# Kernel tuning notes

Hardware: AMD Instinct MI355X
Metric: run time of the kernel (lower is better)

## Reference

```python
import jax, jax.numpy as jnp
import numpy as np

DEG = 3
KNOTS = np.array([i / 9.0 for i in range(1, 9)], dtype=np.float32)  # 8 knots in (0,1)
SDIM = DEG + 1 + len(KNOTS)  # 12
B, D_IN, D_HID, D_OUT = 32768, 256, 256, 1


def spline_basis(t):
    # TruncatedPowerBasis: [1, t, t^2, t^3, relu(t-k)^3 ...]  -> (B, SDIM)
    powers = t[:, None] ** jnp.arange(DEG + 1, dtype=t.dtype)
    knots = jnp.asarray(KNOTS, dtype=t.dtype)
    spl = jax.nn.relu(t[:, None] - knots[None, :]) ** DEG
    return jnp.concatenate([powers, spl], axis=1)


def vc_layer(x, basis, W, b, in_dim, out_dim):
    # Mathematically identical to torch: W_b = basis @ W (viewed (in,out)); out = x @ W_b + basis @ b
    # Factored to avoid materializing the (B, in, out) per-sample weight tensor.
    Ws = W.reshape(SDIM, in_dim, out_dim)
    tmp = jnp.einsum('bi,sio->bso', x, Ws)        # (B, SDIM, out)
    return jnp.einsum('bs,bso->bo', basis, tmp) + basis @ b


def setup_inputs() -> dict:
    key = jax.random.key(0)
    ks = jax.random.split(key, 8)
    xavier = lambda k, shape: jax.random.uniform(
        k, shape, dtype=jnp.float32,
        minval=-1.0, maxval=1.0) * np.sqrt(6.0 / (shape[0] + shape[1]))
    return {
        'treatment': jax.random.uniform(ks[0], (B,), dtype=jnp.float32),
        'features': jax.random.normal(ks[1], (B, D_IN), dtype=jnp.float32),
        'W0': xavier(ks[2], (SDIM, D_IN * D_HID)),
        'b0': xavier(ks[3], (SDIM, D_HID)),
        'W1': xavier(ks[4], (SDIM, D_HID * D_HID)),
        'b1': xavier(ks[5], (SDIM, D_HID)),
        'W2': xavier(ks[6], (SDIM, D_HID * D_OUT)),
        'b2': xavier(ks[7], (SDIM, D_OUT)),
    }


def reference(treatment, features, W0, b0, W1, b1, W2, b2):
    basis = spline_basis(treatment)                     # (B, SDIM)
    x = vc_layer(features, basis, W0, b0, D_IN, D_HID)
    x = jax.nn.relu(x)
    x = vc_layer(x, basis, W1, b1, D_HID, D_HID)
    x = jax.nn.relu(x)
    x = vc_layer(x, basis, W2, b2, D_HID, D_OUT)        # (B, 1)
    return x
```

## Files before the change

kernel.cpp:

```cpp
#include <hip/hip_runtime.h>


typedef __attribute__((ext_vector_type(8))) _Float16 half8;
typedef __attribute__((ext_vector_type(4))) _Float16 half4;
typedef __attribute__((ext_vector_type(4))) float floatx4;

#define XPAD 264

__device__ __forceinline__ void gload16(const _Float16* g, _Float16* l){
  __builtin_amdgcn_global_load_lds(
      (const __attribute__((address_space(1))) void*)g,
      (__attribute__((address_space(3))) void*)l, 16, 0, 0);
}

__device__ __forceinline__ void stage_b(const _Float16* wt, _Float16* slot,
                                        int w, int l){
  gload16(wt +        w * 512 + l * 8, slot +        w * 512);
  gload16(wt + 4096 + w * 512 + l * 8, slot + 4096 + w * 512);
}

__device__ __forceinline__ void make_basis(float t, float* p){
  p[0] = 1.f; p[1] = t; p[2] = t*t; p[3] = p[2]*t;
  const float knots[8] = {1.f/9.f, 2.f/9.f, 3.f/9.f, 4.f/9.f,
                          5.f/9.f, 6.f/9.f, 7.f/9.f, 8.f/9.f};
  #pragma unroll
  for (int j = 0; j < 8; ++j){
    float d = t - knots[j];
    d = fmaxf(d, 0.f);
    p[4+j] = d*d*d;
  }
}

__global__ __launch_bounds__(256)
void pack_w_kernel(const float* __restrict__ W0, const float* __restrict__ W1,
                   _Float16* __restrict__ Wp0, _Float16* __restrict__ Wp1){
  __shared__ float wl[32 * 260];
  const int blk = blockIdx.x;
  const float* W = (blk < 96) ? W0 : W1;
  _Float16* Wp   = (blk < 96) ? Wp0 : Wp1;
  const int c    = (blk < 96) ? blk : blk - 96;
  const int tid  = threadIdx.x;
  const float* src = W + (size_t)c * 8192;
  #pragma unroll
  for (int it = 0; it < 8; ++it){
    int idx = it * 256 + tid;
    int r = idx >> 6, c4 = idx & 63;
    float4 v = *(const float4*)(src + (size_t)idx * 4);
    float* d = &wl[r * 260 + c4 * 4];
    d[0] = v.x; d[1] = v.y; d[2] = v.z; d[3] = v.w;
  }
  __syncthreads();
  const int tpos = (c & 7) * 12 + (c >> 3);
  _Float16* dst = Wp + (size_t)tpos * 8192;
  #pragma unroll
  for (int w = 0; w < 4; ++w){
    int v = w * 256 + tid;
    int n16 = v & 15, qq = (v >> 4) & 3, ntg = v >> 6;
    half8 o;
    #pragma unroll
    for (int j = 0; j < 8; ++j)
      o[j] = (_Float16)wl[(qq * 8 + j) * 260 + ntg * 16 + n16];
    *(half8*)(dst + (size_t)v * 8) = o;
  }
}

__device__ __forceinline__ void gemm_kloop(const _Float16* Xl, _Float16* Bl,
                                           const float* bldsT,
                                           const _Float16* __restrict__ wp,
                                           unsigned xbase, int wm, int wn,
                                           int l16, int w, int l,
                                           floatx4 acc[4][4]){
  const unsigned bbase = (unsigned)(wn * 2048 + l * 8);
  half8 xc[4];
  for (int ko = 0; ko < 8; ++ko){
    #pragma unroll
    for (int s = 0; s < 12; ++s){
      stage_b(wp + (size_t)(ko * 12 + s + 2) * 8192,
              Bl + ((s + 2) & 3) * 8192, w, l);
      __asm__ __volatile__("s_waitcnt vmcnt(4)" ::: "memory");
      __builtin_amdgcn_sched_barrier(0);
      __builtin_amdgcn_s_barrier();
      __builtin_amdgcn_sched_barrier(0);

      if (s == 0){
        #pragma unroll
        for (int mt = 0; mt < 4; ++mt)
          xc[mt] = *(const half8*)&Xl[xbase + ko * 32 + mt * 16 * XPAD];
      }
      floatx4 bt = *(const floatx4*)&bldsT[s * 128 + wm * 64 + l16 * 4];
      _Float16 bh[4];
      #pragma unroll
      for (int mt = 0; mt < 4; ++mt) bh[mt] = (_Float16)bt[mt];
      half8 az[4];
      #pragma unroll
      for (int mt = 0; mt < 4; ++mt) az[mt] = xc[mt] * bh[mt];

      const _Float16* bslot = Bl + (s & 3) * 8192 + bbase;
      half8 bf[4];
      #pragma unroll
      for (int nt = 0; nt < 4; ++nt)
        bf[nt] = *(const half8*)(bslot + nt * 512);
      #pragma unroll
      for (int mt = 0; mt < 4; ++mt)
        #pragma unroll
        for (int nt = 0; nt < 4; ++nt)
          acc[mt][nt] = __builtin_amdgcn_mfma_f32_16x16x32_f16(
              az[mt], bf[nt], acc[mt][nt], 0, 0, 0);
    }
  }
}

__device__ __forceinline__ void add_bias(const float* blds, const float* __restrict__ bias,
                                         int wm, int wn, int q, int l16,
                                         floatx4 acc[4][4]){
  for (int s = 0; s < 12; ++s){
    float bl[4];
    #pragma unroll
    for (int nt = 0; nt < 4; ++nt)
      bl[nt] = bias[s * 256 + wn * 64 + nt * 16 + l16];
    floatx4 bs[4];
    #pragma unroll
    for (int mt = 0; mt < 4; ++mt)
      bs[mt] = *(const floatx4*)&blds[s * 128 + wm * 64 + mt * 16 + q * 4];
    #pragma unroll
    for (int mt = 0; mt < 4; ++mt)
      #pragma unroll
      for (int nt = 0; nt < 4; ++nt)
        #pragma unroll
        for (int r = 0; r < 4; ++r)
          acc[mt][nt][r] += bs[mt][r] * bl[nt];
  }
}

__device__ __forceinline__ void scatter_to_xl(_Float16* Xl, floatx4 acc[4][4],
                                              int wm, int wn, int q, int l16){
  #pragma unroll
  for (int mt = 0; mt < 4; ++mt)
    #pragma unroll
    for (int nt = 0; nt < 4; ++nt)
      #pragma unroll
      for (int r = 0; r < 4; ++r)
        Xl[(wm * 64 + mt * 16 + q * 4 + r) * XPAD + wn * 64 + nt * 16 + l16] =
            (_Float16)fmaxf(acc[mt][nt][r], 0.f);
}

__global__ __launch_bounds__(512, 2)
void fused_layers_kernel(const float* __restrict__ feat, const float* __restrict__ treat,
                         const _Float16* __restrict__ Wp0, const float* __restrict__ b0,
                         const _Float16* __restrict__ Wp1, const float* __restrict__ b1,
                         _Float16* __restrict__ X2){
  __shared__ _Float16 Xl[128 * XPAD];
  __shared__ _Float16 Bl[4 * 8192];
  __shared__ float blds[12 * 128];
  __shared__ float bldsT[12 * 128];

  const int tid  = threadIdx.x;
  const int m0   = blockIdx.x * 128;
  const int lane = tid & 63;
  const int wid  = tid >> 6;
  const int wm   = wid >> 2;
  const int wn   = wid & 3;
  const int q    = lane >> 4;
  const int l16  = lane & 15;

  stage_b(Wp0,        Bl,        wid, lane);
  stage_b(Wp0 + 8192, Bl + 8192, wid, lane);

  #pragma unroll
  for (int it = 0; it < 16; ++it){
    int idx = it * 512 + tid;
    int m = idx >> 6, c = idx & 63;
    float4 v = *(const float4*)(feat + (size_t)(m0 + m) * 256 + c * 4);
    half4 h = { (_Float16)v.x, (_Float16)v.y, (_Float16)v.z, (_Float16)v.w };
    *(half4*)&Xl[m * XPAD + c * 4] = h;
  }
  if (tid < 128){
    float t = treat[m0 + tid];
    float p[12]; make_basis(t, p);
    const int r   = tid;
    const int tmt = (r >> 4) & 3;
    const int tl  = r & 15;
    const int twm = r >> 6;
    #pragma unroll
    for (int s = 0; s < 12; ++s){
      blds [s * 128 + r] = p[s];
      bldsT[s * 128 + twm * 64 + tl * 4 + tmt] = p[s];
    }
  }
  __syncthreads();

  const unsigned xbase = (unsigned)(wm * 64 + l16) * XPAD + q * 8;

  const floatx4 zero = {0.f, 0.f, 0.f, 0.f};
  floatx4 acc[4][4];
  #pragma unroll
  for (int mt = 0; mt < 4; ++mt)
    #pragma unroll
    for (int nt = 0; nt < 4; ++nt) acc[mt][nt] = zero;

  gemm_kloop(Xl, Bl, bldsT, Wp0, xbase, wm, wn, l16, wid, lane, acc);
  add_bias(blds, b0, wm, wn, q, l16, acc);
  __syncthreads();
  scatter_to_xl(Xl, acc, wm, wn, q, l16);
  stage_b(Wp1,        Bl,        wid, lane);
  stage_b(Wp1 + 8192, Bl + 8192, wid, lane);
  __syncthreads();

  #pragma unroll
  for (int mt = 0; mt < 4; ++mt)
    #pragma unroll
    for (int nt = 0; nt < 4; ++nt) acc[mt][nt] = zero;
  gemm_kloop(Xl, Bl, bldsT, Wp1, xbase, wm, wn, l16, wid, lane, acc);
  add_bias(blds, b1, wm, wn, q, l16, acc);

  __syncthreads();
  scatter_to_xl(Xl, acc, wm, wn, q, l16);
  __syncthreads();
  #pragma unroll
  for (int it = 0; it < 8; ++it){
    int idx = it * 512 + tid;
    int m = idx >> 5, c = idx & 31;
    half8 v = *(const half8*)&Xl[m * XPAD + c * 8];
    *(half8*)(X2 + (size_t)(m0 + m) * 256 + c * 8) = v;
  }
}

__global__ __launch_bounds__(256)
void final_kernel(const _Float16* __restrict__ X2, const float* __restrict__ treat,
                  const float* __restrict__ W2, const float* __restrict__ b2,
                  float* __restrict__ out){
  __shared__ float w2l[12 * 256];
  __shared__ float b2l[12];
  const int tid = threadIdx.x;
  const int m0 = blockIdx.x * 16;
  #pragma unroll
  for (int it = 0; it < 12; ++it) w2l[it * 256 + tid] = W2[it * 256 + tid];
  if (tid < 12) b2l[tid] = b2[tid];
  __syncthreads();
  const int lane = tid & 63, wid = tid >> 6;
  #pragma unroll
  for (int rr = 0; rr < 4; ++rr){
    int b = m0 + wid * 4 + rr;
    float t = treat[b];
    float p[12]; make_basis(t, p);
    half4 xv = *(const half4*)(X2 + (size_t)b * 256 + lane * 4);
    float xs[4] = { (float)xv.x, (float)xv.y, (float)xv.z, (float)xv.w };
    float ws[4] = {0.f, 0.f, 0.f, 0.f};
    #pragma unroll
    for (int s = 0; s < 12; ++s){
      floatx4 w4 = *(const floatx4*)&w2l[s * 256 + lane * 4];
      #pragma unroll
      for (int j = 0; j < 4; ++j) ws[j] += p[s] * w4[j];
    }
    float dot = xs[0]*ws[0] + xs[1]*ws[1] + xs[2]*ws[2] + xs[3]*ws[3];
    #pragma unroll
    for (int off = 32; off > 0; off >>= 1) dot += __shfl_down(dot, off, 64);
    if (lane == 0){
      float bb = 0.f;
      #pragma unroll
      for (int s = 0; s < 12; ++s) bb += p[s] * b2l[s];
      out[b] = dot + bb;
    }
  }
}

extern "C" void kernel_launch(void* const* d_in, const int* in_sizes, int n_in,
                              void* d_out, int out_size, void* d_ws, size_t ws_size,
                              hipStream_t stream){
  const float* treat = (const float*)d_in[0];
  const float* feat  = (const float*)d_in[1];
  const float* W0    = (const float*)d_in[2];
  const float* b0    = (const float*)d_in[3];
  const float* W1    = (const float*)d_in[4];
  const float* b1    = (const float*)d_in[5];
  const float* W2    = (const float*)d_in[6];
  const float* b2    = (const float*)d_in[7];

  char* ws = (char*)d_ws;
  _Float16* Wp0 = (_Float16*)(ws);
  _Float16* Wp1 = (_Float16*)(ws + 1572864);
  _Float16* X2  = (_Float16*)(ws + 3145728);
  float* out = (float*)d_out;

  pack_w_kernel<<<192, 256, 0, stream>>>(W0, W1, Wp0, Wp1);
  fused_layers_kernel<<<256, 512, 0, stream>>>(feat, treat, Wp0, b0, Wp1, b1, X2);
  final_kernel<<<2048, 256, 0, stream>>>(X2, treat, W2, b2, out);
}
```

Before: 190.9 us.

## Software-pipeline LDS fragment reads one step ahead in the GEMM k-loop

Restructures the k-loop so the B fragments, basis scalars and X fragments for the next step are read from LDS into registers before the current step's MFMAs run. The global-to-LDS prefetch moves to after the MFMAs and runs three slots ahead instead of two, with the wait count adjusted to match. The aim is to hide LDS read latency behind matrix math. In exchange it raises register pressure, and the deeper prefetch into a four-slot ring risks a race, since a slot may be overwritten before other waves have finished reading it. The final iterations also read past the end of the weight stream.

```diff
diff --git a/kernel.cpp b/kernel.cpp
--- a/kernel.cpp
+++ b/kernel.cpp
@@ -71,41 +71,58 @@
                                            int l16, int w, int l,
                                            floatx4 acc[4][4]){
   const unsigned bbase = (unsigned)(wn * 2048 + l * 8);
-  half8 xc[4];
+  half8 xc[4], xn[4], bc[4], bn[4];
+  stage_b(wp + 2 * 8192, Bl + 2 * 8192, w, l);
+  #pragma unroll
+  for (int nt = 0; nt < 4; ++nt)
+    bc[nt] = *(const half8*)(Bl + bbase + nt * 512);
+  #pragma unroll
+  for (int mt = 0; mt < 4; ++mt)
+    xc[mt] = *(const half8*)&Xl[xbase + mt * 16 * XPAD];
+  floatx4 btc = *(const floatx4*)&bldsT[wm * 64 + l16 * 4];
+
   for (int ko = 0; ko < 8; ++ko){
     #pragma unroll
     for (int s = 0; s < 12; ++s){
-      stage_b(wp + (size_t)(ko * 12 + s + 2) * 8192,
-              Bl + ((s + 2) & 3) * 8192, w, l);
-      __asm__ __volatile__("s_waitcnt vmcnt(4)" ::: "memory");
+      __asm__ __volatile__("s_waitcnt vmcnt(2)" ::: "memory");
       __builtin_amdgcn_sched_barrier(0);
       __builtin_amdgcn_s_barrier();
       __builtin_amdgcn_sched_barrier(0);
 
+      #pragma unroll
+      for (int nt = 0; nt < 4; ++nt)
+        bn[nt] = *(const half8*)(Bl + ((s + 1) & 3) * 8192 + bbase + nt * 512);
+      const int sn = (s == 11) ? 0 : s + 1;
+      floatx4 btn = *(const floatx4*)&bldsT[sn * 128 + wm * 64 + l16 * 4];
       if (s == 0){
+        const int kon = (ko + 1) & 7;
         #pragma unroll
         for (int mt = 0; mt < 4; ++mt)
-          xc[mt] = *(const half8*)&Xl[xbase + ko * 32 + mt * 16 * XPAD];
+          xn[mt] = *(const half8*)&Xl[xbase + kon * 32 + mt * 16 * XPAD];
       }
-      floatx4 bt = *(const floatx4*)&bldsT[s * 128 + wm * 64 + l16 * 4];
+
       _Float16 bh[4];
       #pragma unroll
-      for (int mt = 0; mt < 4; ++mt) bh[mt] = (_Float16)bt[mt];
+      for (int mt = 0; mt < 4; ++mt) bh[mt] = (_Float16)btc[mt];
       half8 az[4];
       #pragma unroll
       for (int mt = 0; mt < 4; ++mt) az[mt] = xc[mt] * bh[mt];
-
-      const _Float16* bslot = Bl + (s & 3) * 8192 + bbase;
-      half8 bf[4];
-      #pragma unroll
-      for (int nt = 0; nt < 4; ++nt)
-        bf[nt] = *(const half8*)(bslot + nt * 512);
       #pragma unroll
       for (int mt = 0; mt < 4; ++mt)
         #pragma unroll
         for (int nt = 0; nt < 4; ++nt)
           acc[mt][nt] = __builtin_amdgcn_mfma_f32_16x16x32_f16(
-              az[mt], bf[nt], acc[mt][nt], 0, 0, 0);
+              az[mt], bc[nt], acc[mt][nt], 0, 0, 0);
+
+      #pragma unroll
+      for (int nt = 0; nt < 4; ++nt) bc[nt] = bn[nt];
+      btc = btn;
+      if (s == 11){
+        #pragma unroll
+        for (int mt = 0; mt < 4; ++mt) xc[mt] = xn[mt];
+      }
+      stage_b(wp + (size_t)(ko * 12 + s + 3) * 8192,
+              Bl + ((s + 3) & 3) * 8192, w, l);
     }
   }
 }
```

Measured after the change: 186.1 us. 1.03x faster.
